# Kernel tuning notes

Measured on AMD Instinct MI355X. Metric: run time of the kernel, lower is better.

Reference implementation:

```python
import jax, jax.numpy as jnp
import numpy as np

B, T, D = 4, 2048, 1024
H, DH = 16, 64

def setup_inputs() -> dict:
    key = jax.random.key(0)
    k1, k2, k3 = jax.random.split(key, 3)
    x = jax.random.normal(k1, (B, T, D), dtype=jnp.float32)
    # nn.Linear weights stored [out, in]; we keep that convention
    w_attn = jax.random.normal(k2, (3 * D, D), dtype=jnp.float32) * (1.0 / np.sqrt(D))
    w_proj = jax.random.normal(k3, (D, D), dtype=jnp.float32) * (1.0 / np.sqrt(D))
    return {"x": x, "w_attn": w_attn, "w_proj": w_proj}

def reference(x, w_attn, w_proj):
    Bx, Tx, Dx = x.shape
    qkv = jnp.einsum('btd,ed->bte', x, w_attn)            # [B,T,3D]
    qkv = qkv.reshape(Bx, Tx, 3, H, DH)
    q = qkv[:, :, 0].transpose(0, 2, 1, 3)                # [B,H,T,DH]
    k = qkv[:, :, 1].transpose(0, 2, 1, 3)
    v = qkv[:, :, 2].transpose(0, 2, 1, 3)
    scale = 1.0 / np.sqrt(DH).astype(np.float32)
    att = jnp.einsum('bhqd,bhkd->bhqk', q, k) * scale     # [B,H,T,T]
    causal = jnp.tril(jnp.ones((Tx, Tx), dtype=bool))
    att = jnp.where(causal[None, None], att, jnp.float32(-jnp.inf))
    att = jax.nn.softmax(att, axis=-1)
    y = jnp.einsum('bhqk,bhkd->bhqd', att, v)             # [B,H,T,DH]
    y = y.transpose(0, 2, 1, 3).reshape(Bx, Tx, Dx)       # [B,T,D]
    y = jnp.einsum('btd,ed->bte', y, w_proj)
    return y
```

## Files before the change

### kernel.cpp

```cpp
#include <hip/hip_runtime.h>

typedef unsigned short u16;
typedef __bf16 bf16x8 __attribute__((ext_vector_type(8)));
typedef float floatx4 __attribute__((ext_vector_type(4)));

__device__ inline u16 f2bf(float x) {
    __bf16 b = (__bf16)x;
    return __builtin_bit_cast(u16, b);
}

__device__ inline floatx4 fzero() {
    floatx4 z = {0.f, 0.f, 0.f, 0.f};
    return z;
}

#if defined(__has_builtin)
#if __has_builtin(__builtin_amdgcn_exp2f)
#define EXP2F(x) __builtin_amdgcn_exp2f(x)
#endif
#endif
#ifndef EXP2F
#define EXP2F(x) exp2f(x)
#endif

template <bool F32>
__device__ inline bf16x8 ld8(const void* base, size_t off) {
    if constexpr (F32) {
        const float* p = (const float*)base + off;
        float4 a = *(const float4*)p;
        float4 b = *(const float4*)(p + 4);
        union { u16 u[8]; bf16x8 v; } t;
        t.u[0] = f2bf(a.x); t.u[1] = f2bf(a.y); t.u[2] = f2bf(a.z); t.u[3] = f2bf(a.w);
        t.u[4] = f2bf(b.x); t.u[5] = f2bf(b.y); t.u[6] = f2bf(b.z); t.u[7] = f2bf(b.w);
        return t.v;
    } else {
        return *(const bf16x8*)((const u16*)base + off);
    }
}

typedef __attribute__((address_space(1))) const unsigned int as1_u32;
typedef __attribute__((address_space(3))) unsigned int as3_u32;
__device__ inline void gld_lds16(const void* g, void* l) {
    __builtin_amdgcn_global_load_lds((as1_u32*)g, (as3_u32*)l, 16, 0, 0);
}

__device__ inline u16* swz_ptr(u16* buf, int row, int col) {
    return (u16*)((char*)buf + row * 128 + ((col * 2) ^ ((row & 7) << 4)));
}

__global__ __launch_bounds__(256) void cvt_all(const float* __restrict__ x,
                                               const float* __restrict__ wa,
                                               const float* __restrict__ wp,
                                               u16* __restrict__ dst) {
    const int XB8 = 1048576, WAB8 = 393216;
    int i = blockIdx.x * 256 + threadIdx.x;
    const float* src; size_t off;
    if (i < XB8)             { src = x;  off = (size_t)i * 8; }
    else if (i < XB8 + WAB8) { src = wa; off = (size_t)(i - XB8) * 8; }
    else                     { src = wp; off = (size_t)(i - XB8 - WAB8) * 8; }
    *(bf16x8*)(dst + (size_t)i * 8) = ld8<true>(src, off);
}

#define BK 32

template <bool AF32, bool BF32, bool CF32>
__global__ __launch_bounds__(256) void gemm_bt(const void* __restrict__ Ap,
                                               const void* __restrict__ Bp,
                                               void* __restrict__ Cp,
                                               int M, int N, int K) {
    __shared__ alignas(16) u16 As[2][128 * BK];
    __shared__ alignas(16) u16 Bs[2][128 * BK];

    const int tid  = threadIdx.x;
    const int lane = tid & 63;
    const int wave = tid >> 6;
    const int wm = (wave >> 1) * 64;
    const int wn = (wave & 1) * 64;
    const int tm = blockIdx.y * 128;
    const int tn = blockIdx.x * 128;
    const int l15 = lane & 15;
    const int l4  = lane >> 4;

    const int srow = tid >> 2;
    const int scol = (tid & 3) * 8;

    floatx4 acc[4][4];
#pragma unroll
    for (int i = 0; i < 4; i++)
#pragma unroll
        for (int j = 0; j < 4; j++) acc[i][j] = fzero();

    if constexpr (!AF32 && !BF32) {
        const u16* Ag = (const u16*)Ap + (size_t)(tm + srow) * K + scol;
        const u16* Bg = (const u16*)Bp + (size_t)(tn + srow) * K + scol;

        auto stage = [&](int buf, int k0) {
            gld_lds16(Ag + k0,                  &As[buf][wave * 512]);
            gld_lds16(Ag + k0 + (size_t)64 * K, &As[buf][2048 + wave * 512]);
            gld_lds16(Bg + k0,                  &Bs[buf][wave * 512]);
            gld_lds16(Bg + k0 + (size_t)64 * K, &Bs[buf][2048 + wave * 512]);
        };

        stage(0, 0);
        __syncthreads();
        int cur = 0;
        const int nk = K / BK;
        for (int t = 0; t < nk; t++) {
            if (t + 1 < nk) stage(cur ^ 1, (t + 1) * BK);

            bf16x8 af[4], bfv[4];
#pragma unroll
            for (int i = 0; i < 4; i++)
                af[i] = *(const bf16x8*)&As[cur][(wm + i * 16 + l15) * BK + l4 * 8];
#pragma unroll
            for (int j = 0; j < 4; j++)
                bfv[j] = *(const bf16x8*)&Bs[cur][(wn + j * 16 + l15) * BK + l4 * 8];
#pragma unroll
            for (int i = 0; i < 4; i++)
#pragma unroll
                for (int j = 0; j < 4; j++)
                    acc[i][j] = __builtin_amdgcn_mfma_f32_16x16x32_bf16(af[i], bfv[j], acc[i][j], 0, 0, 0);

            __syncthreads();
            cur ^= 1;
        }
    } else {
        for (int k0 = 0; k0 < K; k0 += BK) {
            bf16x8 av[2], bv[2];
#pragma unroll
            for (int q = 0; q < 2; q++) {
                av[q] = ld8<AF32>(Ap, (size_t)(tm + srow + q * 64) * K + k0 + scol);
                bv[q] = ld8<BF32>(Bp, (size_t)(tn + srow + q * 64) * K + k0 + scol);
            }
            __syncthreads();
#pragma unroll
            for (int q = 0; q < 2; q++) {
                *(bf16x8*)&As[0][(srow + q * 64) * BK + scol] = av[q];
                *(bf16x8*)&Bs[0][(srow + q * 64) * BK + scol] = bv[q];
            }
            __syncthreads();

            bf16x8 af[4], bfv[4];
#pragma unroll
            for (int i = 0; i < 4; i++)
                af[i] = *(const bf16x8*)&As[0][(wm + i * 16 + l15) * BK + l4 * 8];
#pragma unroll
            for (int j = 0; j < 4; j++)
                bfv[j] = *(const bf16x8*)&Bs[0][(wn + j * 16 + l15) * BK + l4 * 8];
#pragma unroll
            for (int i = 0; i < 4; i++)
#pragma unroll
                for (int j = 0; j < 4; j++)
                    acc[i][j] = __builtin_amdgcn_mfma_f32_16x16x32_bf16(af[i], bfv[j], acc[i][j], 0, 0, 0);
        }
    }

#pragma unroll
    for (int i = 0; i < 4; i++)
#pragma unroll
        for (int j = 0; j < 4; j++)
#pragma unroll
            for (int r = 0; r < 4; r++) {
                int row = tm + wm + i * 16 + l4 * 4 + r;
                int col = tn + wn + j * 16 + l15;
                if constexpr (CF32)
                    ((float*)Cp)[(size_t)row * N + col] = acc[i][j][r];
                else
                    ((u16*)Cp)[(size_t)row * N + col] = f2bf(acc[i][j][r]);
            }
}

__global__ __launch_bounds__(256) void transpose_v(const u16* __restrict__ qkv,
                                                   u16* __restrict__ vT) {
    __shared__ alignas(16) u16 Ts[64 * 80];
    const int bh = blockIdx.x;
    const int b = bh >> 4, h = bh & 15;
    const int t0 = blockIdx.y * 64;
    const int tid = threadIdx.x;
    const int r = tid >> 3;
    const int c = tid & 7;
#pragma unroll
    for (int p = 0; p < 2; p++) {
        int tr = r + p * 32;
        *(bf16x8*)&Ts[tr * 80 + c * 8] =
            *(const bf16x8*)&qkv[(size_t)(b * 2048 + t0 + tr) * 3072 + 2048 + h * 64 + c * 8];
    }
    __syncthreads();
#pragma unroll
    for (int p = 0; p < 2; p++) {
        int dr = r + p * 32;
        union { u16 u[8]; bf16x8 v; } t;
#pragma unroll
        for (int i = 0; i < 8; i++) t.u[i] = Ts[(c * 8 + i) * 80 + dr];
        *(bf16x8*)&vT[(size_t)bh * 131072 + (size_t)dr * 2048 + t0 + c * 8] = t.v;
    }
}

template <bool USE_VT>
__global__ __launch_bounds__(256) void attn2(const u16* __restrict__ qkv,
                                             const u16* __restrict__ vT,
                                             u16* __restrict__ y) {
    const int T = 2048, CW = 3072;
    __shared__ alignas(16) u16 KP[64 * 64];
    __shared__ alignas(16) u16 Vt[64 * 64];
    __shared__ alignas(16) u16 PB[64 * 64];

    const int tid  = threadIdx.x;
    const int lane = tid & 63;
    const int wave = tid >> 6;
    const int l15 = lane & 15;
    const int l4  = lane >> 4;

    const int bh = blockIdx.x;
    const int qt = 31 - blockIdx.y;
    const int b = bh >> 4, h = bh & 15;
    const int q0 = qt * 64;

    const size_t base = (size_t)b * T * CW + h * 64;
    const u16* qp = qkv + base;
    const u16* kp = qkv + base + 1024;
    const u16* vp = qkv + base + 2048;
    const u16* vtp = USE_VT ? (vT + (size_t)bh * 131072) : nullptr;

    bf16x8 qf[2];
    {
        int qrow = q0 + wave * 16 + l15;
        qf[0] = *(const bf16x8*)&qp[(size_t)qrow * CW + l4 * 8];
        qf[1] = *(const bf16x8*)&qp[(size_t)qrow * CW + 32 + l4 * 8];
    }

    bf16x8 ones;
#pragma unroll
    for (int i = 0; i < 8; i++) ones[i] = (__bf16)1.0f;

    const float C2 = 0.18033688f;
    floatx4 Lacc = fzero();
    floatx4 Oacc[4];
#pragma unroll
    for (int cf = 0; cf < 4; cf++) Oacc[cf] = fzero();

    const int sr = tid >> 3;
    const int sc = tid & 7;

    bf16x8 kreg[2], vreg[2];
    auto stage_load = [&](int kt) {
        const int t0 = kt * 64;
#pragma unroll
        for (int p = 0; p < 2; p++)
            kreg[p] = *(const bf16x8*)&kp[(size_t)(t0 + sr + p * 32) * CW + sc * 8];
        if constexpr (USE_VT) {
#pragma unroll
            for (int p = 0; p < 2; p++)
                vreg[p] = *(const bf16x8*)&vtp[(size_t)(sr + p * 32) * 2048 + t0 + sc * 8];
        } else {
            const int dh = tid & 63;
            const int tb = wave * 8;
#pragma unroll
            for (int p = 0; p < 2; p++) {
                union { u16 u[8]; bf16x8 v; } tmp;
#pragma unroll
                for (int i = 0; i < 8; i++)
                    tmp.u[i] = vp[(size_t)(t0 + tb + p * 32 + i) * CW + dh];
                vreg[p] = tmp.v;
            }
        }
    };

    stage_load(0);

    for (int kt = 0; kt <= qt; kt++) {
        const int t0 = kt * 64;
        __syncthreads();

#pragma unroll
        for (int p = 0; p < 2; p++)
            *(bf16x8*)swz_ptr(KP, sr + p * 32, sc * 8) = kreg[p];
        if constexpr (USE_VT) {
#pragma unroll
            for (int p = 0; p < 2; p++)
                *(bf16x8*)swz_ptr(Vt, sr + p * 32, sc * 8) = vreg[p];
        } else {
            const int dh = tid & 63;
            const int tb = wave * 8;
#pragma unroll
            for (int p = 0; p < 2; p++)
                *(bf16x8*)swz_ptr(Vt, dh, tb + p * 32) = vreg[p];
        }
        __syncthreads();

        if (kt < qt) stage_load(kt + 1);

#pragma unroll
        for (int j = 0; j < 4; j++) {
            bf16x8 k0f = *(const bf16x8*)swz_ptr(KP, j * 16 + l15, l4 * 8);
            bf16x8 k1f = *(const bf16x8*)swz_ptr(KP, j * 16 + l15, 32 + l4 * 8);
            floatx4 s = fzero();
            s = __builtin_amdgcn_mfma_f32_16x16x32_bf16(qf[0], k0f, s, 0, 0, 0);
            s = __builtin_amdgcn_mfma_f32_16x16x32_bf16(qf[1], k1f, s, 0, 0, 0);
            float pj[4];
            if (kt == qt) {
#pragma unroll
                for (int r = 0; r < 4; r++) {
                    int qrow = q0 + wave * 16 + l4 * 4 + r;
                    int krow = t0 + j * 16 + l15;
                    float e = (krow <= qrow) ? s[r] * C2 : -1.0e30f;
                    pj[r] = EXP2F(e);
                }
            } else {
#pragma unroll
                for (int r = 0; r < 4; r++) pj[r] = EXP2F(s[r] * C2);
            }
#pragma unroll
            for (int r = 0; r < 4; r++)
                *swz_ptr(PB, wave * 16 + l4 * 4 + r, j * 16 + l15) = f2bf(pj[r]);
        }

        bf16x8 pf0 = *(const bf16x8*)swz_ptr(PB, wave * 16 + l15, l4 * 8);
        bf16x8 pf1 = *(const bf16x8*)swz_ptr(PB, wave * 16 + l15, 32 + l4 * 8);
        Lacc = __builtin_amdgcn_mfma_f32_16x16x32_bf16(pf0, ones, Lacc, 0, 0, 0);
        Lacc = __builtin_amdgcn_mfma_f32_16x16x32_bf16(pf1, ones, Lacc, 0, 0, 0);
#pragma unroll
        for (int cf = 0; cf < 4; cf++) {
            bf16x8 v0f = *(const bf16x8*)swz_ptr(Vt, cf * 16 + l15, l4 * 8);
            bf16x8 v1f = *(const bf16x8*)swz_ptr(Vt, cf * 16 + l15, 32 + l4 * 8);
            Oacc[cf] = __builtin_amdgcn_mfma_f32_16x16x32_bf16(pf0, v0f, Oacc[cf], 0, 0, 0);
            Oacc[cf] = __builtin_amdgcn_mfma_f32_16x16x32_bf16(pf1, v1f, Oacc[cf], 0, 0, 0);
        }
    }

#pragma unroll
    for (int r = 0; r < 4; r++) {
        float inv = 1.0f / Lacc[r];
        int qrow = q0 + wave * 16 + l4 * 4 + r;
        size_t orow = ((size_t)b * T + qrow) * 1024 + h * 64;
#pragma unroll
        for (int cf = 0; cf < 4; cf++)
            y[orow + cf * 16 + l15] = f2bf(Oacc[cf][r] * inv);
    }
}

extern "C" void kernel_launch(void* const* d_in, const int* in_sizes, int n_in,
                              void* d_out, int out_size, void* d_ws, size_t ws_size,
                              hipStream_t stream) {
    const float* x      = (const float*)d_in[0];
    const float* w_attn = (const float*)d_in[1];
    const float* w_proj = (const float*)d_in[2];
    float* out = (float*)d_out;

    const size_t QKV = (size_t)8192 * 3072;
    const size_t Y   = (size_t)8192 * 1024;
    const size_t VTE = (size_t)64 * 64 * 2048;
    const size_t XB  = (size_t)8192 * 1024;
    const size_t WAB = (size_t)3072 * 1024;
    const size_t WPB = (size_t)1024 * 1024;

    u16* qkv = (u16*)d_ws;
    u16* yb  = qkv + QKV;

    const bool full = ws_size >= (QKV + Y + VTE + XB + WAB + WPB) * sizeof(u16);
    const bool mid  = ws_size >= (QKV + Y + VTE) * sizeof(u16);
    if (ws_size < (QKV + Y) * sizeof(u16)) return;

    dim3 blk(256);
    dim3 g1(3072 / 128, 8192 / 128), g2(1024 / 128, 8192 / 128);
    dim3 ga(64, 32);

    if (full) {
        u16* vT  = yb + Y;
        u16* xb  = vT + VTE;
        cvt_all<<<6144, blk, 0, stream>>>(x, w_attn, w_proj, xb);
        u16* wab = xb + XB;
        u16* wpb = wab + WAB;
        gemm_bt<false, false, false><<<g1, blk, 0, stream>>>(xb, wab, qkv, 8192, 3072, 1024);
        transpose_v<<<ga, blk, 0, stream>>>(qkv, vT);
        attn2<true><<<ga, blk, 0, stream>>>(qkv, vT, yb);
        gemm_bt<false, false, true><<<g2, blk, 0, stream>>>(yb, wpb, out, 8192, 1024, 1024);
    } else if (mid) {
        u16* vT = yb + Y;
        gemm_bt<true, true, false><<<g1, blk, 0, stream>>>(x, w_attn, qkv, 8192, 3072, 1024);
        transpose_v<<<ga, blk, 0, stream>>>(qkv, vT);
        attn2<true><<<ga, blk, 0, stream>>>(qkv, vT, yb);
        gemm_bt<false, true, true><<<g2, blk, 0, stream>>>(yb, w_proj, out, 8192, 1024, 1024);
    } else {
        gemm_bt<true, true, false><<<g1, blk, 0, stream>>>(x, w_attn, qkv, 8192, 3072, 1024);
        attn2<false><<<ga, blk, 0, stream>>>(qkv, nullptr, yb);
        gemm_bt<false, true, true><<<g2, blk, 0, stream>>>(yb, w_proj, out, 8192, 1024, 1024);
    }
}
```

Measured before the change: 264.8 us.

## Double-buffer K/V tiles in attention and drop separate V transpose kernel

Removes the standalone transpose_v kernel and its workspace buffer. The attention kernel now loads V directly with strided scalar reads and transposes it in registers. K and V shared-memory tiles are double-buffered, so each iteration needs only one barrier and the next tile's store overlaps with current compute. This saves a kernel launch and one write/read pass over V, but the uncoalesced 2-byte V loads move into the attention kernel's critical loop and the extra LDS buffers may lower occupancy.

Measured after the change: 251.3 us. 5.1% less time.

```diff
diff --git a/kernel.cpp b/kernel.cpp
--- a/kernel.cpp
+++ b/kernel.cpp
@@ -170,39 +170,11 @@
             }
 }
 
-__global__ __launch_bounds__(256) void transpose_v(const u16* __restrict__ qkv,
-                                                   u16* __restrict__ vT) {
-    __shared__ alignas(16) u16 Ts[64 * 80];
-    const int bh = blockIdx.x;
-    const int b = bh >> 4, h = bh & 15;
-    const int t0 = blockIdx.y * 64;
-    const int tid = threadIdx.x;
-    const int r = tid >> 3;
-    const int c = tid & 7;
-#pragma unroll
-    for (int p = 0; p < 2; p++) {
-        int tr = r + p * 32;
-        *(bf16x8*)&Ts[tr * 80 + c * 8] =
-            *(const bf16x8*)&qkv[(size_t)(b * 2048 + t0 + tr) * 3072 + 2048 + h * 64 + c * 8];
-    }
-    __syncthreads();
-#pragma unroll
-    for (int p = 0; p < 2; p++) {
-        int dr = r + p * 32;
-        union { u16 u[8]; bf16x8 v; } t;
-#pragma unroll
-        for (int i = 0; i < 8; i++) t.u[i] = Ts[(c * 8 + i) * 80 + dr];
-        *(bf16x8*)&vT[(size_t)bh * 131072 + (size_t)dr * 2048 + t0 + c * 8] = t.v;
-    }
-}
-
-template <bool USE_VT>
 __global__ __launch_bounds__(256) void attn2(const u16* __restrict__ qkv,
-                                             const u16* __restrict__ vT,
                                              u16* __restrict__ y) {
     const int T = 2048, CW = 3072;
-    __shared__ alignas(16) u16 KP[64 * 64];
-    __shared__ alignas(16) u16 Vt[64 * 64];
+    __shared__ alignas(16) u16 Kb[2][64 * 64];
+    __shared__ alignas(16) u16 Vb[2][64 * 64];
     __shared__ alignas(16) u16 PB[64 * 64];
 
     const int tid  = threadIdx.x;
@@ -220,7 +192,6 @@
     const u16* qp = qkv + base;
     const u16* kp = qkv + base + 1024;
     const u16* vp = qkv + base + 2048;
-    const u16* vtp = USE_VT ? (vT + (size_t)bh * 131072) : nullptr;
 
     bf16x8 qf[2];
     {
@@ -241,6 +212,8 @@
 
     const int sr = tid >> 3;
     const int sc = tid & 7;
+    const int dh = lane;
+    const int tb = wave * 8;
 
     bf16x8 kreg[2], vreg[2];
     auto stage_load = [&](int kt) {
@@ -248,47 +221,35 @@
 #pragma unroll
         for (int p = 0; p < 2; p++)
             kreg[p] = *(const bf16x8*)&kp[(size_t)(t0 + sr + p * 32) * CW + sc * 8];
-        if constexpr (USE_VT) {
-#pragma unroll
-            for (int p = 0; p < 2; p++)
-                vreg[p] = *(const bf16x8*)&vtp[(size_t)(sr + p * 32) * 2048 + t0 + sc * 8];
-        } else {
-            const int dh = tid & 63;
-            const int tb = wave * 8;
-#pragma unroll
-            for (int p = 0; p < 2; p++) {
-                union { u16 u[8]; bf16x8 v; } tmp;
-#pragma unroll
-                for (int i = 0; i < 8; i++)
-                    tmp.u[i] = vp[(size_t)(t0 + tb + p * 32 + i) * CW + dh];
-                vreg[p] = tmp.v;
-            }
+#pragma unroll
+        for (int p = 0; p < 2; p++) {
+            union { u16 u[8]; bf16x8 v; } tmp;
+#pragma unroll
+            for (int i = 0; i < 8; i++)
+                tmp.u[i] = vp[(size_t)(t0 + tb + p * 32 + i) * CW + dh];
+            vreg[p] = tmp.v;
         }
     };
 
+    auto commit = [&](int buf) {
+#pragma unroll
+        for (int p = 0; p < 2; p++)
+            *(bf16x8*)swz_ptr(&Kb[buf][0], sr + p * 32, sc * 8) = kreg[p];
+#pragma unroll
+        for (int p = 0; p < 2; p++)
+            *(bf16x8*)swz_ptr(&Vb[buf][0], dh, tb + p * 32) = vreg[p];
+    };
+
     stage_load(0);
+    commit(0);
+    if (qt >= 1) stage_load(1);
+    __syncthreads();
 
     for (int kt = 0; kt <= qt; kt++) {
         const int t0 = kt * 64;
-        __syncthreads();
-
-#pragma unroll
-        for (int p = 0; p < 2; p++)
-            *(bf16x8*)swz_ptr(KP, sr + p * 32, sc * 8) = kreg[p];
-        if constexpr (USE_VT) {
-#pragma unroll
-            for (int p = 0; p < 2; p++)
-                *(bf16x8*)swz_ptr(Vt, sr + p * 32, sc * 8) = vreg[p];
-        } else {
-            const int dh = tid & 63;
-            const int tb = wave * 8;
-#pragma unroll
-            for (int p = 0; p < 2; p++)
-                *(bf16x8*)swz_ptr(Vt, dh, tb + p * 32) = vreg[p];
-        }
-        __syncthreads();
-
-        if (kt < qt) stage_load(kt + 1);
+        const int cur = kt & 1;
+        u16* KP = &Kb[cur][0];
+        u16* Vt = &Vb[cur][0];
 
 #pragma unroll
         for (int j = 0; j < 4; j++) {
@@ -326,6 +287,10 @@
             Oacc[cf] = __builtin_amdgcn_mfma_f32_16x16x32_bf16(pf0, v0f, Oacc[cf], 0, 0, 0);
             Oacc[cf] = __builtin_amdgcn_mfma_f32_16x16x32_bf16(pf1, v1f, Oacc[cf], 0, 0, 0);
         }
+
+        if (kt + 1 <= qt) commit(cur ^ 1);
+        if (kt + 2 <= qt) stage_load(kt + 2);
+        __syncthreads();
     }
 
 #pragma unroll
@@ -349,7 +314,6 @@
 
     const size_t QKV = (size_t)8192 * 3072;
     const size_t Y   = (size_t)8192 * 1024;
-    const size_t VTE = (size_t)64 * 64 * 2048;
     const size_t XB  = (size_t)8192 * 1024;
     const size_t WAB = (size_t)3072 * 1024;
     const size_t WPB = (size_t)1024 * 1024;
@@ -357,8 +321,7 @@
     u16* qkv = (u16*)d_ws;
     u16* yb  = qkv + QKV;
 
-    const bool full = ws_size >= (QKV + Y + VTE + XB + WAB + WPB) * sizeof(u16);
-    const bool mid  = ws_size >= (QKV + Y + VTE) * sizeof(u16);
+    const bool full = ws_size >= (QKV + Y + XB + WAB + WPB) * sizeof(u16);
     if (ws_size < (QKV + Y) * sizeof(u16)) return;
 
     dim3 blk(256);
@@ -366,24 +329,16 @@
     dim3 ga(64, 32);
 
     if (full) {
-        u16* vT  = yb + Y;
-        u16* xb  = vT + VTE;
+        u16* xb  = yb + Y;
         cvt_all<<<6144, blk, 0, stream>>>(x, w_attn, w_proj, xb);
         u16* wab = xb + XB;
         u16* wpb = wab + WAB;
         gemm_bt<false, false, false><<<g1, blk, 0, stream>>>(xb, wab, qkv, 8192, 3072, 1024);
-        transpose_v<<<ga, blk, 0, stream>>>(qkv, vT);
-        attn2<true><<<ga, blk, 0, stream>>>(qkv, vT, yb);
+        attn2<<<ga, blk, 0, stream>>>(qkv, yb);
         gemm_bt<false, false, true><<<g2, blk, 0, stream>>>(yb, wpb, out, 8192, 1024, 1024);
-    } else if (mid) {
-        u16* vT = yb + Y;
-        gemm_bt<true, true, false><<<g1, blk, 0, stream>>>(x, w_attn, qkv, 8192, 3072, 1024);
-        transpose_v<<<ga, blk, 0, stream>>>(qkv, vT);
-        attn2<true><<<ga, blk, 0, stream>>>(qkv, vT, yb);
-        gemm_bt<false, true, true><<<g2, blk, 0, stream>>>(yb, w_proj, out, 8192, 1024, 1024);
     } else {
         gemm_bt<true, true, false><<<g1, blk, 0, stream>>>(x, w_attn, qkv, 8192, 3072, 1024);
-        attn2<false><<<ga, blk, 0, stream>>>(qkv, nullptr, yb);
+        attn2<<<ga, blk, 0, stream>>>(qkv, yb);
         gemm_bt<false, true, true><<<g2, blk, 0, stream>>>(yb, w_proj, out, 8192, 1024, 1024);
     }
 }
```
